# Kernel optimization log

Measured on AMD Instinct MI355X. Metric: run time of the kernel, lower is better.

The kernel has to match this reference:

```python
import jax, jax.numpy as jnp
import numpy as np

D_MODEL = 128
D_STATE = 64
L = 1024
BATCH = 32
DT_MIN, DT_MAX = 1e-3, 1e-1

# poly6 Chebyshev coeffs for GELU on domain [-5, 15]
POLY6_GELU = [6.04831644882, 8.094460228971, 1.371512430522, -0.740775295685,
              0.134773988002, 0.126019270103, -0.239569101196]
GELU_LO, GELU_HI = -5.0, 15.0


def cheb_eval(x, coeffs, lo, hi):
    t = (2.0 * x - (hi + lo)) / (hi - lo)
    t0 = jnp.ones_like(t)
    res = coeffs[0] * t0
    t1 = t
    res = res + coeffs[1] * t1
    for i in range(2, len(coeffs)):
        ti = 2.0 * t * t1 - t0
        res = res + coeffs[i] * ti
        t0, t1 = t1, ti
    return res


def setup_inputs() -> dict:
    key = jax.random.key(0)
    ks = jax.random.split(key, 8)
    u = jax.random.normal(ks[0], (BATCH, D_MODEL, L), dtype=jnp.float32)
    # S4DKernel params
    log_dt = jax.random.uniform(ks[1], (D_MODEL,), dtype=jnp.float32) * (np.log(DT_MAX) - np.log(DT_MIN)) + np.log(DT_MIN)
    log_A_real = jnp.log(0.5 * jnp.ones((D_MODEL, D_STATE), dtype=jnp.float32))
    A_imag = jnp.pi * jnp.tile(jnp.arange(D_STATE, dtype=jnp.float32), (D_MODEL, 1))
    B_re = jnp.ones((D_MODEL, D_STATE), dtype=jnp.float32)
    B_im = jnp.zeros((D_MODEL, D_STATE), dtype=jnp.float32)
    C_re = jax.random.normal(ks[2], (D_MODEL, D_STATE), dtype=jnp.float32)
    C_im = jax.random.normal(ks[3], (D_MODEL, D_STATE), dtype=jnp.float32)
    # block params
    D = jax.random.normal(ks[4], (D_MODEL,), dtype=jnp.float32)
    W1 = jax.random.normal(ks[5], (2 * D_MODEL, D_MODEL), dtype=jnp.float32) * (1.0 / np.sqrt(D_MODEL))
    b1 = jnp.zeros((2 * D_MODEL,), dtype=jnp.float32)
    Wdec = jax.random.normal(ks[6], (1, D_MODEL), dtype=jnp.float32) * (1.0 / np.sqrt(D_MODEL))
    bdec = jnp.zeros((1,), dtype=jnp.float32)
    return {"u": u, "log_dt": log_dt, "log_A_real": log_A_real, "A_imag": A_imag,
            "B_re": B_re, "B_im": B_im, "C_re": C_re, "C_im": C_im,
            "D": D, "W1": W1, "b1": b1, "Wdec": Wdec, "bdec": bdec}


def s4d_kernel(log_dt, log_A_real, A_imag, B_re, B_im, C_re, C_im, length):
    dt = jnp.exp(log_dt)                                  # (d,)
    A = -jnp.exp(log_A_real) + 1j * A_imag                # (d, n) complex
    A_bar = jnp.exp(A * dt[:, None])                      # (d, n)
    Bc = B_re + 1j * B_im
    Cc = C_re + 1j * C_im
    B_bar = (A_bar - 1.0) / A * Bc                        # (d, n)
    t = jnp.arange(length, dtype=jnp.float32)
    # A_bar ** t for integer t == exp(A * dt * t)  (branch cut cancels at integers)
    A_bar_pow = jnp.exp((A * dt[:, None])[:, :, None] * t)  # (d, n, L)
    K = jnp.sum(Cc[:, :, None] * A_bar_pow * B_bar[:, :, None], axis=1)  # (d, L)
    return jnp.real(K).astype(jnp.float32)


def reference(u, log_dt, log_A_real, A_imag, B_re, B_im, C_re, C_im, D, W1, b1, Wdec, bdec):
    d_model = u.shape[1]
    length = u.shape[2]
    K = s4d_kernel(log_dt, log_A_real, A_imag, B_re, B_im, C_re, C_im, length)  # (d, L)
    # torch F.conv1d(padding=L-1, groups=d)[..., :L] == left-padded depthwise cross-correlation
    conv = jax.lax.conv_general_dilated(
        u, K[:, None, :], window_strides=(1,), padding=[(length - 1, 0)],
        dimension_numbers=("NCH", "OIH", "NCH"), feature_group_count=d_model)  # (B, d, L)
    skip = conv + u * D[:, None]
    post_gelu = cheb_eval(skip, POLY6_GELU, GELU_LO, GELU_HI)
    # 1x1 conv to 2*d channels
    pre_gate = jnp.einsum("od,bdl->bol", W1, post_gelu) + b1[None, :, None]  # (B, 2d, L)
    a, b = jnp.split(pre_gate, 2, axis=1)
    gate = jnp.clip(0.25 * b + 0.5, 0.0, 1.0)  # linear_gate GLU
    gated = a * gate                            # (B, d, L)
    pooled = gated.mean(axis=-1)                # (B, d)
    return pooled @ Wdec.T + bdec               # (B, 1)
```

## Files before the change

kernel.cpp:

```cpp
#include <hip/hip_runtime.h>
#include <hip/hip_bf16.h>
#include <math.h>

#define D_MODEL 128
#define D_STATE 64
#define LEN 1024
#define BATCH 32
#define KROW 1064
#define KC_STRIDE 1056

typedef short short8 __attribute__((ext_vector_type(8)));
typedef short short4v __attribute__((ext_vector_type(4)));
typedef float f32x4 __attribute__((ext_vector_type(4)));
typedef float f32x16 __attribute__((ext_vector_type(16)));
typedef float float4u __attribute__((ext_vector_type(4), aligned(4)));

__device__ __forceinline__ float gelu_cheb(float x) {
    float t = (2.0f * x - 10.0f) * 0.05f;
    float r = 6.04831644882f + 8.094460228971f * t;
    float tm1 = 1.0f, tc = t;
    float t2 = 2.0f * t * tc - tm1; r += 1.371512430522f  * t2;
    float t3 = 2.0f * t * t2 - tc;  r += -0.740775295685f * t3;
    float t4 = 2.0f * t * t3 - t2;  r += 0.134773988002f  * t4;
    float t5 = 2.0f * t * t4 - t3;  r += 0.126019270103f  * t5;
    float t6 = 2.0f * t * t5 - t4;  r += -0.239569101196f * t6;
    return r;
}

__device__ __forceinline__ unsigned f2bf(float f) {
    unsigned u = __float_as_uint(f);
    return (u + 0x7FFFu + ((u >> 16) & 1u)) >> 16;
}

__device__ __forceinline__ float bf2f(short s) {
    return __uint_as_float(((unsigned)(unsigned short)s) << 16);
}

__global__ __launch_bounds__(256) void k_genK4(const float* __restrict__ log_dt,
                                               const float* __restrict__ log_A_real,
                                               const float* __restrict__ A_imag,
                                               const float* __restrict__ B_re,
                                               const float* __restrict__ B_im,
                                               const float* __restrict__ C_re,
                                               const float* __restrict__ C_im,
                                               const float* __restrict__ W1,
                                               const float* __restrict__ u,
                                               short* __restrict__ w1bf,
                                               short* __restrict__ u_bfT,
                                               float* __restrict__ K) {
    __shared__ float Ls[128][68];
    __shared__ __align__(16) short Ut[4096];
    int bid = blockIdx.x;
    int d = bid >> 3, oct = bid & 7;
    int t = threadIdx.x;

    if (t < 32) { int i = bid * 32 + t; w1bf[i] = (short)f2bf(W1[i]); }

    {
        int r = t >> 3, c8 = t & 7;
        const float* up = u + ((size_t)(r * D_MODEL + d) << 10) + oct * 128 + c8 * 16;
        float4 a  = *(const float4*)(up);
        float4 b4 = *(const float4*)(up + 4);
        float4 c4 = *(const float4*)(up + 8);
        float4 d4 = *(const float4*)(up + 12);
        uint4 o0, o1;
        o0.x = f2bf(a.x)  | (f2bf(a.y)  << 16);
        o0.y = f2bf(a.z)  | (f2bf(a.w)  << 16);
        o0.z = f2bf(b4.x) | (f2bf(b4.y) << 16);
        o0.w = f2bf(b4.z) | (f2bf(b4.w) << 16);
        o1.x = f2bf(c4.x) | (f2bf(c4.y) << 16);
        o1.y = f2bf(c4.z) | (f2bf(c4.w) << 16);
        o1.z = f2bf(d4.x) | (f2bf(d4.y) << 16);
        o1.w = f2bf(d4.z) | (f2bf(d4.w) << 16);
        int jcl = 2 * c8;
        *(uint4*)&Ut[(jcl * 32 + r) * 8]       = o0;
        *(uint4*)&Ut[((jcl + 1) * 32 + r) * 8] = o1;
    }

    int w = t >> 6, lane = t & 63;
    int idx = d * D_STATE + lane;
    float dt  = expf(log_dt[d]);
    float Are = -expf(log_A_real[idx]);
    float Aim = A_imag[idx];
    float dre = Are * dt, dim = Aim * dt;
    float e = expf(dre);
    float sn, cs; sincosf(dim, &sn, &cs);
    float zre = e * cs, zim = e * sn;
    float numr = zre - 1.0f, numi = zim;
    float inv = 1.0f / (Are * Are + Aim * Aim);
    float qr = (numr * Are + numi * Aim) * inv;
    float qi = (numi * Are - numr * Aim) * inv;
    float Br = B_re[idx], Bi = B_im[idx];
    float Bbr = qr * Br - qi * Bi;
    float Bbi = qr * Bi + qi * Br;
    float Cr = C_re[idx], Ci = C_im[idx];
    float ar = Cr * Bbr - Ci * Bbi;
    float ai = Cr * Bbi + Ci * Bbr;

    int L0 = oct * 128 + w * 32;
    float fl0 = (float)L0;
    float pre = 0.f, pim = 0.f;
    if (dre * fl0 > -30.f) {
        float e0 = expf(dre * fl0);
        float s0, c0; sincosf(dim * fl0, &s0, &c0);
        pre = e0 * (ar * c0 - ai * s0);
        pim = e0 * (ar * s0 + ai * c0);
    }

    int row0 = w * 32;
#pragma unroll
    for (int r = 0; r < 32; ++r) {
        Ls[row0 + r][lane] = pre;
        float nre = pre * zre - pim * zim;
        pim = pre * zim + pim * zre;
        pre = nre;
    }
    __syncthreads();

    {
        uint4* dst = (uint4*)(u_bfT + (size_t)d * 32768 + oct * 4096) + t * 2;
        const uint4* srcl = (const uint4*)Ut + t * 2;
        dst[0] = srcl[0]; dst[1] = srcl[1];
    }

    if (t < 128) {
        f32x4 s4 = (f32x4){0.f, 0.f, 0.f, 0.f};
#pragma unroll
        for (int c = 0; c < 16; ++c) s4 += *(const f32x4*)&Ls[t][4 * c];
        K[(size_t)d * KROW + oct * 128 + t] = s4.x + s4.y + s4.z + s4.w;
    } else if (oct == 7 && t < 168) {
        K[(size_t)d * KROW + 1024 + (t - 128)] = 0.f;
    }
}

__global__ __launch_bounds__(256) void k_conv8(const float* __restrict__ K,
                                               const short* __restrict__ u_bfT,
                                               const float* __restrict__ Dp,
                                               short* __restrict__ pgT) {
    __shared__ __align__(16) short Kc[8 * KC_STRIDE];
    __shared__ __align__(16) short Us[64 * 256];
    int bid = blockIdx.x;
    int d   = bid >> 2;
    int e   = (bid >> 1) & 1;
    int ph2 = bid & 1;
    int t = threadIdx.x;

    {
        const float* kp = K + (size_t)d * KROW;
        int c = t >> 5;
        short* outp = Kc + c * KC_STRIDE;
        for (int i = (t & 31); i < 132; i += 32) {
            float4u a = *(const float4u*)(kp + 8 * i + c);
            float4u b = *(const float4u*)(kp + 8 * i + c + 4);
            uint4 o;
            o.x = f2bf(a.x) | (f2bf(a.y) << 16);
            o.y = f2bf(a.z) | (f2bf(a.w) << 16);
            o.z = f2bf(b.x) | (f2bf(b.y) << 16);
            o.w = f2bf(b.z) | (f2bf(b.w) << 16);
            *(uint4*)(outp + 8 * i) = o;
        }
    }
    const uint4* usrc = (const uint4*)(u_bfT + ((size_t)d << 15));
    {
        uint4* dstl = (uint4*)Us;
        for (int v = t; v < 2048; v += 256) dstl[v] = usrc[v];
    }
    __syncthreads();

    int w = __builtin_amdgcn_readfirstlane(t >> 6);
    int lane = t & 63;
    int mm = lane & 31, h = lane >> 5;
    int cc = (7 - mm) & 7;
    const short* Krow = Kc + cc * KC_STRIDE;
    const short* bbase = Us + mm * 8 + h * 256;

    int P = 30 + 2 * e;
    int p = e + 2 * (4 * ph2 + w);
    int q = P - p;
    int xb = 1023 + 8 * h - mm - cc;
    int xp = xb - 32 * p;
    int xq = xb - 32 * q;

    f32x16 accs[2];
#pragma unroll
    for (int i = 0; i < 16; ++i) { accs[0][i] = 0.f; accs[1][i] = 0.f; }

    int tp = 2 * p + 2;
    for (int ks = 0; ks < 32; ++ks) {
        short8 bfrag = *(const short8*)(bbase + ks * 512);
        short8 a1 = *(const short8*)&Krow[xq + 16 * ks];
        accs[1] = __builtin_amdgcn_mfma_f32_32x32x16_bf16(a1, bfrag, accs[1], 0, 0, 0);
        if (ks < tp) {
            short8 a2 = *(const short8*)&Krow[xp + 16 * ks];
            accs[0] = __builtin_amdgcn_mfma_f32_32x32x16_bf16(a2, bfrag, accs[0], 0, 0, 0);
        }
    }
    __syncthreads();
    {
        uint4* dstl = (uint4*)Us;
        for (int v = t; v < 2048; v += 256) dstl[v] = usrc[v + 2048];
    }
    __syncthreads();
    int tq = 2 * q - 30;
    for (int ks2 = 0; ks2 < tq; ++ks2) {
        short8 bfrag = *(const short8*)(bbase + ks2 * 512);
        short8 a1 = *(const short8*)&Krow[xq + 16 * (32 + ks2)];
        accs[1] = __builtin_amdgcn_mfma_f32_32x32x16_bf16(a1, bfrag, accs[1], 0, 0, 0);
    }

    float Dd = Dp[d];
#pragma unroll
    for (int c2 = 0; c2 < 2; ++c2) {
        int I = c2 ? q : p;
        size_t pbase = ((size_t)mm * LEN + 32 * I) * D_MODEL + d;
#pragma unroll
        for (int rg = 0; rg < 4; ++rg) {
            int lofs = 8 * rg + 4 * h;
            const short* sp = u_bfT + ((size_t)d << 15) + (4 * I + rg) * 256 + mm * 8 + 4 * h;
            short4v us = *(const short4v*)sp;
#pragma unroll
            for (int rr = 0; rr < 4; ++rr) {
                float v = gelu_cheb(accs[c2][rg * 4 + rr] + bf2f(us[rr]) * Dd);
                pgT[pbase + (size_t)(lofs + rr) * D_MODEL] = (short)f2bf(v);
            }
        }
    }
}

__global__ __launch_bounds__(256) void k_glu_mfma(const short* __restrict__ pgT,
                                                  const short* __restrict__ w1bf,
                                                  const float* __restrict__ b1,
                                                  const float* __restrict__ Wdec,
                                                  float* __restrict__ acc2) {
    __shared__ float red[4];
    int b = blockIdx.y;
    int lc = blockIdx.x;
    int l0 = lc * 64;
    int t = threadIdx.x;
    int wv = t >> 6, lane = t & 63;
    int m = lane & 15, q = lane >> 4;

    const short* wA0 = w1bf + ((2 * wv + 0) * 16 + m) * D_MODEL;
    const short* wA1 = w1bf + ((2 * wv + 1) * 16 + m) * D_MODEL;

    short8 aA0[4], aA1[4], aB0[4], aB1[4];
#pragma unroll
    for (int kki = 0; kki < 4; ++kki) {
        int ko = kki * 32 + q * 8;
        aA0[kki] = *(const short8*)(wA0 + ko);
        aA1[kki] = *(const short8*)(wA1 + ko);
        aB0[kki] = *(const short8*)(wA0 + 128 * D_MODEL + ko);
        aB1[kki] = *(const short8*)(wA1 + 128 * D_MODEL + ko);
    }

    const short* pgb = pgT + ((size_t)b * LEN + l0) * D_MODEL;

    f32x4 accA[2][4], accB[2][4];
#pragma unroll
    for (int p = 0; p < 2; ++p)
#pragma unroll
        for (int nt = 0; nt < 4; ++nt) {
            accA[p][nt] = (f32x4){0.f, 0.f, 0.f, 0.f};
            accB[p][nt] = (f32x4){0.f, 0.f, 0.f, 0.f};
        }

#pragma unroll
    for (int kki = 0; kki < 4; ++kki) {
        int ko = kki * 32 + q * 8;
        short8 bfr[4];
#pragma unroll
        for (int nt = 0; nt < 4; ++nt)
            bfr[nt] = *(const short8*)&pgb[(size_t)(nt * 16 + m) * D_MODEL + ko];
#pragma unroll
        for (int nt = 0; nt < 4; ++nt) {
            accA[0][nt] = __builtin_amdgcn_mfma_f32_16x16x32_bf16(aA0[kki], bfr[nt], accA[0][nt], 0, 0, 0);
            accA[1][nt] = __builtin_amdgcn_mfma_f32_16x16x32_bf16(aA1[kki], bfr[nt], accA[1][nt], 0, 0, 0);
            accB[0][nt] = __builtin_amdgcn_mfma_f32_16x16x32_bf16(aB0[kki], bfr[nt], accB[0][nt], 0, 0, 0);
            accB[1][nt] = __builtin_amdgcn_mfma_f32_16x16x32_bf16(aB1[kki], bfr[nt], accB[1][nt], 0, 0, 0);
        }
    }

    float s = 0.f;
#pragma unroll
    for (int p = 0; p < 2; ++p) {
        int oA = (2 * wv + p) * 16 + q * 4;
#pragma unroll
        for (int r = 0; r < 4; ++r) {
            int o = oA + r;
            float wd  = Wdec[o];
            float ba  = b1[o];
            float bb1 = b1[o + 128];
#pragma unroll
            for (int nt = 0; nt < 4; ++nt) {
                float aa  = accA[p][nt][r] + ba;
                float bbv = accB[p][nt][r] + bb1;
                float g = fminf(fmaxf(0.25f * bbv + 0.5f, 0.f), 1.f);
                s += wd * aa * g;
            }
        }
    }
#pragma unroll
    for (int off = 32; off > 0; off >>= 1) s += __shfl_down(s, off, 64);
    if (lane == 0) red[wv] = s;
    __syncthreads();
    if (t == 0) acc2[b * 16 + lc] = red[0] + red[1] + red[2] + red[3];
}

__global__ void k_finish(const float* __restrict__ acc2, const float* __restrict__ bdec,
                         float* __restrict__ out) {
    int b = threadIdx.x;
    if (b < BATCH) {
        float s = 0.f;
#pragma unroll
        for (int c = 0; c < 16; ++c) s += acc2[b * 16 + c];
        out[b] = s * (1.0f / (float)LEN) + bdec[0];
    }
}

extern "C" void kernel_launch(void* const* d_in, const int* in_sizes, int n_in,
                              void* d_out, int out_size, void* d_ws, size_t ws_size,
                              hipStream_t stream) {
    const float* u          = (const float*)d_in[0];
    const float* log_dt     = (const float*)d_in[1];
    const float* log_A_real = (const float*)d_in[2];
    const float* A_imag     = (const float*)d_in[3];
    const float* B_re       = (const float*)d_in[4];
    const float* B_im       = (const float*)d_in[5];
    const float* C_re       = (const float*)d_in[6];
    const float* C_im       = (const float*)d_in[7];
    const float* Dp         = (const float*)d_in[8];
    const float* W1         = (const float*)d_in[9];
    const float* b1         = (const float*)d_in[10];
    const float* Wdec       = (const float*)d_in[11];
    const float* bdec       = (const float*)d_in[12];
    float* out = (float*)d_out;

    float* w = (float*)d_ws;
    float* K      = w;
    float* acc2   = K + (size_t)D_MODEL * KROW;
    short* u_bfT  = (short*)(acc2 + 512);
    short* pgT    = u_bfT + (size_t)BATCH * D_MODEL * LEN;
    short* w1bf   = pgT + (size_t)BATCH * LEN * D_MODEL;

    k_genK4<<<D_MODEL * 8, 256, 0, stream>>>(log_dt, log_A_real, A_imag, B_re, B_im,
                                             C_re, C_im, W1, u, w1bf, u_bfT, K);
    k_conv8<<<512, 256, 0, stream>>>(K, u_bfT, Dp, pgT);
    k_glu_mfma<<<dim3(16, BATCH), 256, 0, stream>>>(pgT, w1bf, b1, Wdec, acc2);
    k_finish<<<1, 64, 0, stream>>>(acc2, bdec, out);
}
```

Measured before the change: 137.1 us.

## Store post-GELU activations channel-major and transpose through LDS in GLU kernel

```diff
diff --git a/kernel.cpp b/kernel.cpp
--- a/kernel.cpp
+++ b/kernel.cpp
@@ -133,10 +133,10 @@
     }
 }
 
-__global__ __launch_bounds__(256) void k_conv8(const float* __restrict__ K,
+__global__ __launch_bounds__(256) void k_conv9(const float* __restrict__ K,
                                                const short* __restrict__ u_bfT,
                                                const float* __restrict__ Dp,
-                                               short* __restrict__ pgT) {
+                                               short* __restrict__ pg2) {
     __shared__ __align__(16) short Kc[8 * KC_STRIDE];
     __shared__ __align__(16) short Us[64 * 256];
     int bid = blockIdx.x;
@@ -212,31 +212,50 @@
 #pragma unroll
     for (int c2 = 0; c2 < 2; ++c2) {
         int I = c2 ? q : p;
-        size_t pbase = ((size_t)mm * LEN + 32 * I) * D_MODEL + d;
+        size_t rowb = ((size_t)(mm * D_MODEL + d) << 10) + 32 * I;
 #pragma unroll
         for (int rg = 0; rg < 4; ++rg) {
-            int lofs = 8 * rg + 4 * h;
             const short* sp = u_bfT + ((size_t)d << 15) + (4 * I + rg) * 256 + mm * 8 + 4 * h;
             short4v us = *(const short4v*)sp;
+            short4v pk;
 #pragma unroll
             for (int rr = 0; rr < 4; ++rr) {
                 float v = gelu_cheb(accs[c2][rg * 4 + rr] + bf2f(us[rr]) * Dd);
-                pgT[pbase + (size_t)(lofs + rr) * D_MODEL] = (short)f2bf(v);
+                pk[rr] = (short)f2bf(v);
             }
-        }
-    }
-}
-
-__global__ __launch_bounds__(256) void k_glu_mfma(const short* __restrict__ pgT,
-                                                  const short* __restrict__ w1bf,
-                                                  const float* __restrict__ b1,
-                                                  const float* __restrict__ Wdec,
-                                                  float* __restrict__ acc2) {
+            *(short4v*)(pg2 + rowb + 8 * rg + 4 * h) = pk;
+        }
+    }
+}
+
+__global__ __launch_bounds__(256) void k_glu2(const short* __restrict__ pg2,
+                                              const short* __restrict__ w1bf,
+                                              const float* __restrict__ b1,
+                                              const float* __restrict__ Wdec,
+                                              float* __restrict__ acc2) {
+    __shared__ __align__(16) short xs[64 * 136];
     __shared__ float red[4];
     int b = blockIdx.y;
     int lc = blockIdx.x;
     int l0 = lc * 64;
     int t = threadIdx.x;
+
+    {
+        int dp = t & 63, lq = t >> 6;
+        const short* r0 = pg2 + (((size_t)b * D_MODEL + 2 * dp) << 10) + l0 + lq * 16;
+        short8 a0 = *(const short8*)r0;
+        short8 a1 = *(const short8*)(r0 + 8);
+        short8 c0 = *(const short8*)(r0 + 1024);
+        short8 c1 = *(const short8*)(r0 + 1032);
+#pragma unroll
+        for (int i = 0; i < 8; ++i) {
+            *(unsigned*)&xs[(lq * 16 + i) * 136 + 2 * dp] =
+                (unsigned)(unsigned short)a0[i] | ((unsigned)(unsigned short)c0[i] << 16);
+            *(unsigned*)&xs[(lq * 16 + 8 + i) * 136 + 2 * dp] =
+                (unsigned)(unsigned short)a1[i] | ((unsigned)(unsigned short)c1[i] << 16);
+        }
+    }
+
     int wv = t >> 6, lane = t & 63;
     int m = lane & 15, q = lane >> 4;
 
@@ -252,8 +271,7 @@
         aB0[kki] = *(const short8*)(wA0 + 128 * D_MODEL + ko);
         aB1[kki] = *(const short8*)(wA1 + 128 * D_MODEL + ko);
     }
-
-    const short* pgb = pgT + ((size_t)b * LEN + l0) * D_MODEL;
+    __syncthreads();
 
     f32x4 accA[2][4], accB[2][4];
 #pragma unroll
@@ -270,7 +288,7 @@
         short8 bfr[4];
 #pragma unroll
         for (int nt = 0; nt < 4; ++nt)
-            bfr[nt] = *(const short8*)&pgb[(size_t)(nt * 16 + m) * D_MODEL + ko];
+            bfr[nt] = *(const short8*)&xs[(nt * 16 + m) * 136 + ko];
 #pragma unroll
         for (int nt = 0; nt < 4; ++nt) {
             accA[0][nt] = __builtin_amdgcn_mfma_f32_16x16x32_bf16(aA0[kki], bfr[nt], accA[0][nt], 0, 0, 0);
@@ -339,12 +357,12 @@
     float* K      = w;
     float* acc2   = K + (size_t)D_MODEL * KROW;
     short* u_bfT  = (short*)(acc2 + 512);
-    short* pgT    = u_bfT + (size_t)BATCH * D_MODEL * LEN;
-    short* w1bf   = pgT + (size_t)BATCH * LEN * D_MODEL;
+    short* pg2    = u_bfT + (size_t)BATCH * D_MODEL * LEN;
+    short* w1bf   = pg2 + (size_t)BATCH * LEN * D_MODEL;
 
     k_genK4<<<D_MODEL * 8, 256, 0, stream>>>(log_dt, log_A_real, A_imag, B_re, B_im,
                                              C_re, C_im, W1, u, w1bf, u_bfT, K);
-    k_conv8<<<512, 256, 0, stream>>>(K, u_bfT, Dp, pgT);
-    k_glu_mfma<<<dim3(16, BATCH), 256, 0, stream>>>(pgT, w1bf, b1, Wdec, acc2);
+    k_conv9<<<512, 256, 0, stream>>>(K, u_bfT, Dp, pg2);
+    k_glu2<<<dim3(16, BATCH), 256, 0, stream>>>(pg2, w1bf, b1, Wdec, acc2);
     k_finish<<<1, 64, 0, stream>>>(acc2, bdec, out);
 }
```

Result: faster. 114.8 us (median of 2 runs) (-16.2%).
